# Kernel tuning notes

Hardware: AMD Instinct MI355X
Metric: run time of the kernel (lower is better)

## Reference

```python
import math
import jax, jax.numpy as jnp
import numpy as np

B, T_BI, D_BI = 64, 3000, 128
T_SW, D_SW = 375, 192
T_S1, D_S1 = 188, 192
N_FIRES = 300          # static fire count (target_lengths all = 300 -> beta = 1, ceil(sum)=300)
D_MODEL = 512
SCALE = 4.0            # scale_factor
EPS_LN = 1e-5


def _cif_integrate(h, alpha, thr, n_fires):
    """Vectorized CIF: cumsum + two scatter-adds (matches torch _cif_forward).
    h [B,T,D], alpha [B,T], thr [B,1] -> [B,n_fires,D]."""
    Bq, T, D = h.shape
    a = alpha / thr                       # normalize so boundaries sit at integers
    c = jnp.cumsum(a, axis=1)
    prev = c - a
    kp = jnp.floor(prev)
    kc = jnp.floor(c)
    fired = kc > kp                       # frame crosses a token boundary
    w_hi = jnp.where(fired, (c - kc) * thr, 0.0)          # leftover into new token
    w_lo = jnp.where(fired, (kp + 1.0 - prev) * thr, alpha)  # portion completing old token
    ip = jnp.clip(kp.astype(jnp.int32), 0, n_fires - 1)
    ic = jnp.clip(kc.astype(jnp.int32), 0, n_fires - 1)
    bidx = jnp.broadcast_to(jnp.arange(Bq)[:, None], (Bq, T))
    out = jnp.zeros((Bq, n_fires, D), h.dtype)
    out = out.at[bidx, ip].add(w_lo[..., None] * h)
    out = out.at[bidx, ic].add(w_hi[..., None] * h)
    return out


def _interp(src, t_cont, t_bi):
    """Linear interp of src [B,Ts,D] at continuous fire times t_cont [B,N] (given on the T_bi grid)."""
    Bq, Ts, D = src.shape
    t = t_cont * Ts / t_bi
    lo = jnp.clip(t.astype(jnp.int32), 0, Ts - 2)
    w = (t - lo.astype(t.dtype))[..., None]
    idx_lo = jnp.broadcast_to(lo[..., None], (Bq, t.shape[1], D))
    g_lo = jnp.take_along_axis(src, idx_lo, axis=1)
    g_hi = jnp.take_along_axis(src, idx_lo + 1, axis=1)
    return (1.0 - w) * g_lo + w * g_hi


def _forward(fire_signal, acoustic_src, acoustic_src_s1, conv_w, ln_g, ln_b, wp_w, wp_b,
             film_s0_w, film_s0_b, film_s1_w, film_s1_b, tproj_w, tproj_b,
             aproj_w, aproj_b, bproj_w, bproj_b, target_lengths):
    Bq, T_bi, _ = fire_signal.shape
    # 1) weight predictor: depthwise conv (k=1, no bias) -> LN -> Linear -> sigmoid
    x = fire_signal * conv_w                                   # depthwise 1x1 conv
    mu = jnp.mean(x, axis=-1, keepdims=True)
    var = jnp.var(x, axis=-1, keepdims=True)
    xn = (x - mu) * jax.lax.rsqrt(var + EPS_LN) * ln_g + ln_b
    alpha = SCALE * jax.nn.sigmoid(xn @ wp_w + wp_b)           # [B,T]
    tgt = target_lengths.astype(alpha.dtype)
    qty_loss = jnp.mean(jnp.abs(jnp.sum(alpha, axis=1) - tgt))
    # training-mode alpha normalization (sum alpha_cif == target)
    sum_a = jnp.clip(jnp.sum(alpha, axis=1, keepdims=True), 1e-8)
    alpha_cif = alpha * (tgt[:, None] / sum_a)
    # dynamic threshold beta = sum / ceil(sum)  (== 1 here since targets are integers)
    sum_cif = jnp.sum(alpha_cif, axis=1)
    ceil_sum = jax.lax.stop_gradient(jnp.clip(jnp.ceil(sum_cif), 1.0))
    thr = (sum_cif / ceil_sum)[:, None]                        # [B,1]
    # 2) CIF integration of temporal channel
    acoustic_temporal = _cif_integrate(fire_signal, alpha_cif, thr, N_FIRES)  # [B,N,128]
    # continuous fire times
    cum = jnp.cumsum(alpha_cif, axis=1)
    thresholds = jnp.arange(1, N_FIRES + 1, dtype=alpha.dtype)[None, :] * thr  # [B,N]
    ff = jax.vmap(jnp.searchsorted)(cum, thresholds)
    ff = jnp.minimum(ff, T_bi - 1)
    t_lo = jnp.maximum(ff - 1, 0)
    cum_at = jnp.take_along_axis(cum, t_lo, axis=1)
    a_at = jnp.take_along_axis(alpha_cif, ff, axis=1)
    t_cont = t_lo.astype(alpha.dtype) + (thresholds - cum_at) / jnp.clip(a_at, 1e-8)
    t_cont = jnp.clip(t_cont, 0.0, T_bi - 1)
    # 3) S0 pitch channel: interp + FiLM
    acoustic_pitch = _interp(acoustic_src, t_cont, T_bi)       # [B,N,192]
    film0 = acoustic_temporal @ film_s0_w + film_s0_b
    g0, b0 = jnp.split(film0, 2, axis=-1)
    pitch_mod = g0 * acoustic_pitch + b0
    # 4) project + combine
    embs = (acoustic_temporal @ tproj_w + tproj_b) + (pitch_mod @ aproj_w + aproj_b)
    # S1 beat channel
    acoustic_beat = _interp(acoustic_src_s1, t_cont, T_bi)     # [B,N,192]
    film1 = acoustic_temporal @ film_s1_w + film_s1_b
    g1, b1 = jnp.split(film1, 2, axis=-1)
    beat_mod = g1 * acoustic_beat + b1
    embs = embs + (beat_mod @ bproj_w + bproj_b)
    return embs, alpha, qty_loss


def setup_inputs() -> dict:
    key = jax.random.key(0)
    ks = jax.random.split(key, 14)
    # weight_proj bias init per module: alpha_init = target_fires/encoder_len
    p = min((128.0 / 3000.0) / SCALE, 0.99)
    wp_bias = math.log(p / (1.0 - p))
    f32 = jnp.float32
    return {
        "fire_signal": jax.random.normal(ks[0], (B, T_BI, D_BI), f32),
        "acoustic_src": jax.random.normal(ks[1], (B, T_SW, D_SW), f32),
        "acoustic_src_s1": jax.random.normal(ks[2], (B, T_S1, D_S1), f32),
        "target_lengths": jnp.full((B,), N_FIRES, jnp.int32),
        "conv_w": 1.0 + 0.1 * jax.random.normal(ks[3], (D_BI,), f32),
        "ln_g": jnp.ones((D_BI,), f32),
        "ln_b": jnp.zeros((D_BI,), f32),
        "wp_w": 0.02 * jax.random.normal(ks[4], (D_BI,), f32),
        "wp_b": jnp.asarray(wp_bias, f32),
        "film_s0_w": 0.02 * jax.random.normal(ks[5], (D_BI, 2 * D_SW), f32),
        "film_s0_b": jnp.concatenate([jnp.ones((D_SW,), f32), jnp.zeros((D_SW,), f32)]),
        "film_s1_w": 0.02 * jax.random.normal(ks[6], (D_BI, 2 * D_S1), f32),
        "film_s1_b": jnp.concatenate([jnp.ones((D_S1,), f32), jnp.zeros((D_S1,), f32)]),
        "tproj_w": 0.02 * jax.random.normal(ks[7], (D_BI, D_MODEL), f32),
        "tproj_b": jnp.zeros((D_MODEL,), f32),
        "aproj_w": 0.02 * jax.random.normal(ks[8], (D_SW, D_MODEL), f32),
        "aproj_b": jnp.zeros((D_MODEL,), f32),
        "bproj_w": 0.02 * jax.random.normal(ks[9], (D_S1, D_MODEL), f32),
        "bproj_b": jnp.zeros((D_MODEL,), f32),
    }


def reference(fire_signal, acoustic_src, acoustic_src_s1, target_lengths, conv_w, ln_g, ln_b,
              wp_w, wp_b, film_s0_w, film_s0_b, film_s1_w, film_s1_b, tproj_w, tproj_b,
              aproj_w, aproj_b, bproj_w, bproj_b):
    return _forward(fire_signal, acoustic_src, acoustic_src_s1, conv_w, ln_g, ln_b, wp_w, wp_b,
                    film_s0_w, film_s0_b, film_s1_w, film_s1_b, tproj_w, tproj_b,
                    aproj_w, aproj_b, bproj_w, bproj_b, target_lengths)
```

## Files before the change

### kernel.cpp

```cpp
#include <hip/hip_runtime.h>
#include <math.h>

#define BQ 64
#define TBI 3000
#define DBI 128
#define TSW 375
#define TS1 188
#define DSW 192
#define NF 300
#define DMODEL 512
#define EPSLN 1e-5f

typedef __bf16 bf16x8 __attribute__((ext_vector_type(8)));
typedef float f32x4 __attribute__((ext_vector_type(4)));

__device__ __forceinline__ unsigned short f2bf(float f) {
    unsigned u = __float_as_uint(f);
    unsigned r = (u + 0x7FFFu + ((u >> 16) & 1u)) >> 16;
    return (unsigned short)r;
}

__global__ __launch_bounds__(256) void k_alpha2(
    const float* __restrict__ fs, const float* __restrict__ conv_w,
    const float* __restrict__ ln_g, const float* __restrict__ ln_b,
    const float* __restrict__ wp_w, const float* __restrict__ wp_b,
    float* __restrict__ alpha_out)
{
    int wave = threadIdx.x >> 6, lane = threadIdx.x & 63;
    int l = lane & 31;
    long g = (long)blockIdx.x * 8 + wave * 2 + (lane >> 5);
    const float* row = fs + g * DBI;
    float4 f  = *(const float4*)&row[4 * l];
    float4 cw = *(const float4*)&conv_w[4 * l];
    float4 x; x.x = f.x * cw.x; x.y = f.y * cw.y; x.z = f.z * cw.z; x.w = f.w * cw.w;
    float s = x.x + x.y + x.z + x.w;
    for (int m = 16; m >= 1; m >>= 1) s += __shfl_xor(s, m, 64);
    float mu = s * (1.0f / 128.0f);
    float4 d; d.x = x.x - mu; d.y = x.y - mu; d.z = x.z - mu; d.w = x.w - mu;
    float q = d.x * d.x + d.y * d.y + d.z * d.z + d.w * d.w;
    for (int m = 16; m >= 1; m >>= 1) q += __shfl_xor(q, m, 64);
    float var = q * (1.0f / 128.0f);
    float rs = rsqrtf(var + EPSLN);
    float4 lg = *(const float4*)&ln_g[4 * l];
    float4 lb = *(const float4*)&ln_b[4 * l];
    float4 wp = *(const float4*)&wp_w[4 * l];
    float z = (d.x * rs * lg.x + lb.x) * wp.x + (d.y * rs * lg.y + lb.y) * wp.y
            + (d.z * rs * lg.z + lb.z) * wp.z + (d.w * rs * lg.w + lb.w) * wp.w;
    for (int m = 16; m >= 1; m >>= 1) z += __shfl_xor(z, m, 64);
    z += wp_b[0];
    float a = 4.0f / (1.0f + expf(-z));
    if (l == 0) alpha_out[g] = a;
}

__global__ __launch_bounds__(1024) void k_scan2(
    const float* __restrict__ alpha, const int* __restrict__ tlen,
    float2* __restrict__ params, float* __restrict__ qtyb,
    float2* __restrict__ c2, float* __restrict__ tcont)
{
    __shared__ float2 sc[TBI];
    __shared__ float2 part[2][1024];
    __shared__ double red[1024];
    int b = blockIdx.x, tid = threadIdx.x;
    const float* ar = alpha + (long)b * TBI;
    double s = 0.0;
    for (int t = tid; t < TBI; t += 1024) s += (double)ar[t];
    red[tid] = s; __syncthreads();
    for (int d = 512; d >= 1; d >>= 1) { if (tid < d) red[tid] += red[tid + d]; __syncthreads(); }
    double sum_a = red[0]; __syncthreads();
    double tgt = (double)tlen[b];
    double sa = sum_a < 1e-8 ? 1e-8 : sum_a;
    float r = (float)(tgt / sa);
    double s2 = 0.0;
    for (int t = tid; t < TBI; t += 1024) s2 += (double)(ar[t] * r);
    red[tid] = s2; __syncthreads();
    for (int d = 512; d >= 1; d >>= 1) { if (tid < d) red[tid] += red[tid + d]; __syncthreads(); }
    float sum_cif = (float)red[0];
    float cs = ceilf(sum_cif); if (cs < 1.0f) cs = 1.0f;
    float thr = sum_cif / cs;
    float rthr = 1.0f / thr;
    if (tid == 0) { params[b] = make_float2(r, thr); qtyb[b] = (float)fabs(sum_a - tgt); }
    int base = tid * 3;
    float2 run = make_float2(0.f, 0.f);
    if (base < TBI) {
        for (int j = 0; j < 3; ++j) {
            int t = base + j;
            float ac = ar[t] * r;
            run.x += ac * rthr; run.y += ac;
            sc[t] = run;
        }
    }
    part[0][tid] = (base < TBI) ? run : make_float2(0.f, 0.f);
    __syncthreads();
    int srcb = 0;
    for (int d = 1; d < 1024; d <<= 1) {
        float2 v = part[srcb][tid];
        if (tid >= d) { float2 u = part[srcb][tid - d]; v.x += u.x; v.y += u.y; }
        part[srcb ^ 1][tid] = v;
        srcb ^= 1;
        __syncthreads();
    }
    if (base < TBI && tid > 0) {
        float2 off = part[srcb][tid - 1];
        for (int j = 0; j < 3; ++j) { sc[base + j].x += off.x; sc[base + j].y += off.y; }
    }
    __syncthreads();
    for (int t = tid; t < TBI; t += 1024) {
        float ac = ar[t] * r;
        c2[(long)b * TBI + t] = make_float2(sc[t].x, ac);
    }
    if (tid < NF) {
        float v = (float)(tid + 1) * thr;
        int lo = 0, hi = TBI;
        while (lo < hi) { int mid = (lo + hi) >> 1; if (sc[mid].y < v) lo = mid + 1; else hi = mid; }
        int ff = lo; if (ff > TBI - 1) ff = TBI - 1;
        int tl = ff - 1; if (tl < 0) tl = 0;
        float cum_at = sc[tl].y;
        float a_at = ar[ff] * r;
        if (a_at < 1e-8f) a_at = 1e-8f;
        float tc = (float)tl + (v - cum_at) / a_at;
        tc = fminf(fmaxf(tc, 0.0f), (float)(TBI - 1));
        tcont[b * NF + tid] = tc;
    }
}

__global__ void k_qty(const float* __restrict__ qtyb, float* __restrict__ out)
{
    float v = qtyb[threadIdx.x & 63];
    for (int m = 32; m >= 1; m >>= 1) v += __shfl_xor(v, m, 64);
    if (threadIdx.x == 0) out[0] = v * (1.0f / (float)BQ);
}

#define FPW 94
__global__ __launch_bounds__(256) void k_cif2(
    const float* __restrict__ fs, const float2* __restrict__ c2,
    const float2* __restrict__ params, float* __restrict__ at)
{
    int wid = threadIdx.x >> 6, lane = threadIdx.x & 63;
    int wg = blockIdx.x * 4 + wid;
    int b = wg >> 5, slot = wg & 31;
    int t0 = slot * FPW;
    int t1 = t0 + FPW; if (t1 > TBI) t1 = TBI;
    if (t0 >= t1) return;
    float thr = params[b].y;
    float rthr = 1.0f / thr;
    const float2* cb = c2 + (long)b * TBI;
    const float* fb = fs + (long)b * TBI * DBI;
    float* ab = at + (long)b * NF * DBI;
    int cur = -1;
    float a0 = 0.f, a1 = 0.f;
    float2 v = cb[t0];
    float2 h = *(const float2*)&fb[(long)t0 * DBI + 2 * lane];
    for (int t = t0; t < t1; ++t) {
        float2 vn = v, hn = h;
        if (t + 1 < t1) {
            vn = cb[t + 1];
            hn = *(const float2*)&fb[(long)(t + 1) * DBI + 2 * lane];
        }
        float c = v.x, ac = v.y;
        float av = ac * rthr;
        float prev = c - av;
        float kp = floorf(prev), kc = floorf(c);
        bool fired = kc > kp;
        float w_lo = fired ? (kp + 1.0f - prev) * thr : ac;
        float w_hi = fired ? (c - kc) * thr : 0.0f;
        int ip = (int)kp; if (ip > NF - 1) ip = NF - 1; if (ip < 0) ip = 0;
        int ic = (int)kc; if (ic > NF - 1) ic = NF - 1; if (ic < 0) ic = 0;
        if (ip != cur) {
            if (cur >= 0) { atomicAdd(&ab[cur * DBI + 2 * lane], a0); atomicAdd(&ab[cur * DBI + 2 * lane + 1], a1); }
            cur = ip; a0 = 0.f; a1 = 0.f;
        }
        a0 += w_lo * h.x; a1 += w_lo * h.y;
        if (fired) {
            if (ic != cur) {
                if (cur >= 0) { atomicAdd(&ab[cur * DBI + 2 * lane], a0); atomicAdd(&ab[cur * DBI + 2 * lane + 1], a1); }
                cur = ic; a0 = 0.f; a1 = 0.f;
            }
            a0 += w_hi * h.x; a1 += w_hi * h.y;
        }
        v = vn; h = hn;
    }
    if (cur >= 0) { atomicAdd(&ab[cur * DBI + 2 * lane], a0); atomicAdd(&ab[cur * DBI + 2 * lane + 1], a1); }
}

__global__ __launch_bounds__(256) void k_prep(
    const float* __restrict__ f0w, const float* __restrict__ f1w,
    const float* __restrict__ tw, const float* __restrict__ aw, const float* __restrict__ bw,
    unsigned short* __restrict__ Wg, unsigned short* __restrict__ Wb,
    unsigned short* __restrict__ W2)
{
    int i = blockIdx.x * 256 + threadIdx.x;
    if (i < 49152) {
        int j = i & 7, lane = (i >> 3) & 63, kt = (i >> 9) & 3, nt = i >> 11;
        int k = kt * 32 + (lane >> 4) * 8 + j;
        int n = nt * 16 + (lane & 15);
        float g, b;
        if (n < 192) { g = f0w[k * 384 + n];         b = f0w[k * 384 + n + 192]; }
        else         { g = f1w[k * 384 + (n - 192)]; b = f1w[k * 384 + (n - 192) + 192]; }
        Wg[i] = f2bf(g); Wb[i] = f2bf(b);
    } else if (i < 49152 + 262144) {
        int ii = i - 49152;
        int j = ii & 7, lane = (ii >> 3) & 63, kt = (ii >> 9) & 15, nt = ii >> 13;
        int k = kt * 32 + (lane >> 4) * 8 + j;
        int n = nt * 16 + (lane & 15);
        float v;
        if (k < 128)      v = tw[k * 512 + n];
        else if (k < 320) v = aw[(k - 128) * 512 + n];
        else              v = bw[(k - 320) * 512 + n];
        W2[ii] = f2bf(v);
    }
}

__global__ void k_prepb(const float* __restrict__ f0b, const float* __restrict__ f1b,
                        const float* __restrict__ tb, const float* __restrict__ apb,
                        const float* __restrict__ bpb,
                        float* __restrict__ gbias, float* __restrict__ bbias,
                        float* __restrict__ bias2)
{
    int c = threadIdx.x;
    if (c < 384) {
        gbias[c] = c < 192 ? f0b[c] : f1b[c - 192];
        bbias[c] = c < 192 ? f0b[c + 192] : f1b[c - 192 + 192];
    }
    bias2[c] = tb[c] + apb[c] + bpb[c];
}

#define ROWS 32
__global__ __launch_bounds__(512) void k_emb4(
    const float* __restrict__ at, const float* __restrict__ tcont,
    const float* __restrict__ src0, const float* __restrict__ src1,
    const unsigned short* __restrict__ Wg, const unsigned short* __restrict__ Wb,
    const unsigned short* __restrict__ W2,
    const float* __restrict__ gbias, const float* __restrict__ bbias,
    const float* __restrict__ bias2, float* __restrict__ embs)
{
    __shared__ __align__(16) unsigned short X[ROWS][520];
    __shared__ float s_w0[ROWS], s_w1[ROWS];
    __shared__ int s_lo0[ROWS], s_lo1[ROWS], s_b[ROWS];
    int tid = threadIdx.x;
    int wave = tid >> 6, lane = tid & 63;
    long r0 = (long)blockIdx.x * ROWS;
    for (int idx = tid; idx < ROWS * 32; idx += 512) {
        int r = idx >> 5, k4 = (idx & 31) * 4;
        float4 v = *(const float4*)&at[(r0 + r) * DBI + k4];
        X[r][k4 + 0] = f2bf(v.x); X[r][k4 + 1] = f2bf(v.y);
        X[r][k4 + 2] = f2bf(v.z); X[r][k4 + 3] = f2bf(v.w);
    }
    if (tid < ROWS) {
        long g = r0 + tid;
        s_b[tid] = (int)(g / NF);
        float tc = tcont[g];
        float t0 = tc * ((float)TSW / 3000.0f);
        int lo0 = (int)t0; if (lo0 > TSW - 2) lo0 = TSW - 2; if (lo0 < 0) lo0 = 0;
        s_lo0[tid] = lo0; s_w0[tid] = t0 - (float)lo0;
        float t1 = tc * ((float)TS1 / 3000.0f);
        int lo1 = (int)t1; if (lo1 > TS1 - 2) lo1 = TS1 - 2; if (lo1 < 0) lo1 = 0;
        s_lo1[tid] = lo1; s_w1[tid] = t1 - (float)lo1;
    }
    __syncthreads();
    int mrow = lane & 15, quad = lane >> 4;
    for (int nt = wave; nt < 24; nt += 8) {
        f32x4 ag0 = {0,0,0,0}, ag1 = {0,0,0,0}, ab0 = {0,0,0,0}, ab1 = {0,0,0,0};
        #pragma unroll
        for (int kt = 0; kt < 4; ++kt) {
            bf16x8 a0 = *(const bf16x8*)&X[mrow][kt * 32 + quad * 8];
            bf16x8 a1 = *(const bf16x8*)&X[16 + mrow][kt * 32 + quad * 8];
            bf16x8 bg = *(const bf16x8*)&Wg[(((nt * 4 + kt) * 64) + lane) * 8];
            bf16x8 bb = *(const bf16x8*)&Wb[(((nt * 4 + kt) * 64) + lane) * 8];
            ag0 = __builtin_amdgcn_mfma_f32_16x16x32_bf16(a0, bg, ag0, 0, 0, 0);
            ag1 = __builtin_amdgcn_mfma_f32_16x16x32_bf16(a1, bg, ag1, 0, 0, 0);
            ab0 = __builtin_amdgcn_mfma_f32_16x16x32_bf16(a0, bb, ab0, 0, 0, 0);
            ab1 = __builtin_amdgcn_mfma_f32_16x16x32_bf16(a1, bb, ab1, 0, 0, 0);
        }
        int c = nt * 16 + mrow;
        bool sel = c >= DSW;
        int cc = sel ? c - DSW : c;
        const float* S = sel ? src1 : src0;
        int Ts = sel ? TS1 : TSW;
        float gb = gbias[c], bbv = bbias[c];
        #pragma unroll
        for (int m = 0; m < 2; ++m) {
            #pragma unroll
            for (int q = 0; q < 4; ++q) {
                int r = m * 16 + quad * 4 + q;
                int b = s_b[r];
                int lo = sel ? s_lo1[r] : s_lo0[r];
                float w = sel ? s_w1[r] : s_w0[r];
                const float* Sp = S + ((long)b * Ts + lo) * DSW + cc;
                float pv = (1.0f - w) * Sp[0] + w * Sp[DSW];
                float gv = (m ? ag1[q] : ag0[q]) + gb;
                float bv = (m ? ab1[q] : ab0[q]) + bbv;
                X[r][128 + c] = f2bf(gv * pv + bv);
            }
        }
    }
    __syncthreads();
    f32x4 acc0[4], acc1[4];
    #pragma unroll
    for (int n = 0; n < 4; ++n) { acc0[n] = (f32x4){0,0,0,0}; acc1[n] = (f32x4){0,0,0,0}; }
    for (int kt = 0; kt < 16; ++kt) {
        bf16x8 a0 = *(const bf16x8*)&X[mrow][kt * 32 + quad * 8];
        bf16x8 a1 = *(const bf16x8*)&X[16 + mrow][kt * 32 + quad * 8];
        #pragma unroll
        for (int n = 0; n < 4; ++n) {
            int nt = wave * 4 + n;
            bf16x8 bfv = *(const bf16x8*)&W2[((nt * 16 + kt) * 64 + lane) * 8];
            acc0[n] = __builtin_amdgcn_mfma_f32_16x16x32_bf16(a0, bfv, acc0[n], 0, 0, 0);
            acc1[n] = __builtin_amdgcn_mfma_f32_16x16x32_bf16(a1, bfv, acc1[n], 0, 0, 0);
        }
    }
    #pragma unroll
    for (int n = 0; n < 4; ++n) {
        int cbase = (wave * 4 + n) * 16 + mrow;
        float bv = bias2[cbase];
        #pragma unroll
        for (int q = 0; q < 4; ++q) {
            embs[(r0 + quad * 4 + q) * DMODEL + cbase] = acc0[n][q] + bv;
            embs[(r0 + 16 + quad * 4 + q) * DMODEL + cbase] = acc1[n][q] + bv;
        }
    }
}

extern "C" void kernel_launch(void* const* d_in, const int* in_sizes, int n_in,
                              void* d_out, int out_size, void* d_ws, size_t ws_size,
                              hipStream_t stream)
{
    const float* fs     = (const float*)d_in[0];
    const float* src0   = (const float*)d_in[1];
    const float* src1   = (const float*)d_in[2];
    const int*   tlen   = (const int*)d_in[3];
    const float* conv_w = (const float*)d_in[4];
    const float* ln_g   = (const float*)d_in[5];
    const float* ln_b   = (const float*)d_in[6];
    const float* wp_w   = (const float*)d_in[7];
    const float* wp_b   = (const float*)d_in[8];
    const float* f0w    = (const float*)d_in[9];
    const float* f0b    = (const float*)d_in[10];
    const float* f1w    = (const float*)d_in[11];
    const float* f1b    = (const float*)d_in[12];
    const float* tw     = (const float*)d_in[13];
    const float* tb     = (const float*)d_in[14];
    const float* aw     = (const float*)d_in[15];
    const float* apb    = (const float*)d_in[16];
    const float* bw     = (const float*)d_in[17];
    const float* bpb    = (const float*)d_in[18];

    float* embs  = (float*)d_out;
    float* alpha = embs + (long)BQ * NF * DMODEL;
    float* qtyo  = alpha + (long)BQ * TBI;

    char* ws = (char*)d_ws;
    size_t off = 0;
    float*  at     = (float*)(ws + off);  off += 9830400;
    float2* c2     = (float2*)(ws + off); off += 1536000;
    float*  tcont  = (float*)(ws + off);  off += 76800;
    float2* params = (float2*)(ws + off); off += 512;
    float*  qtyb   = (float*)(ws + off);  off += 256;
    unsigned short* Wg = (unsigned short*)(ws + off); off += 98304;
    unsigned short* Wb = (unsigned short*)(ws + off); off += 98304;
    unsigned short* W2 = (unsigned short*)(ws + off); off += 524288;
    float* gbias = (float*)(ws + off); off += 1536;
    float* bbias = (float*)(ws + off); off += 1536;
    float* bias2 = (float*)(ws + off); off += 2048;

    hipMemsetAsync(at, 0, (size_t)BQ * NF * DBI * sizeof(float), stream);
    k_prep<<<1216, 256, 0, stream>>>(f0w, f1w, tw, aw, bw, Wg, Wb, W2);
    k_prepb<<<1, 512, 0, stream>>>(f0b, f1b, tb, apb, bpb, gbias, bbias, bias2);
    k_alpha2<<<(BQ * TBI) / 8, 256, 0, stream>>>(fs, conv_w, ln_g, ln_b, wp_w, wp_b, alpha);
    k_scan2<<<BQ, 1024, 0, stream>>>(alpha, tlen, params, qtyb, c2, tcont);
    k_qty<<<1, 64, 0, stream>>>(qtyb, qtyo);
    k_cif2<<<512, 256, 0, stream>>>(fs, c2, params, at);
    k_emb4<<<(BQ * NF) / ROWS, 512, 0, stream>>>(at, tcont, src0, src1,
                                                 Wg, Wb, W2, gbias, bbias, bias2, embs);
}
```

Baseline: 297.4 us.

## Partition CIF by output tokens to drop atomics and memset, merge small launches

```diff
diff --git a/kernel.cpp b/kernel.cpp
--- a/kernel.cpp
+++ b/kernel.cpp
@@ -52,10 +52,10 @@
     if (l == 0) alpha_out[g] = a;
 }
 
-__global__ __launch_bounds__(1024) void k_scan2(
+__global__ __launch_bounds__(1024) void k_scan3(
     const float* __restrict__ alpha, const int* __restrict__ tlen,
-    float2* __restrict__ params, float* __restrict__ qtyb,
-    float2* __restrict__ c2, float* __restrict__ tcont)
+    float2* __restrict__ params, float* __restrict__ qtyo,
+    float2* __restrict__ c2, float* __restrict__ tcont, int* __restrict__ ffout)
 {
     __shared__ float2 sc[TBI];
     __shared__ float2 part[2][1024];
@@ -78,7 +78,10 @@
     float cs = ceilf(sum_cif); if (cs < 1.0f) cs = 1.0f;
     float thr = sum_cif / cs;
     float rthr = 1.0f / thr;
-    if (tid == 0) { params[b] = make_float2(r, thr); qtyb[b] = (float)fabs(sum_a - tgt); }
+    if (tid == 0) {
+        params[b] = make_float2(r, thr);
+        atomicAdd(qtyo, (float)fabs(sum_a - tgt) * (1.0f / (float)BQ));
+    }
     int base = tid * 3;
     float2 run = make_float2(0.f, 0.f);
     if (base < TBI) {
@@ -113,6 +116,7 @@
         int lo = 0, hi = TBI;
         while (lo < hi) { int mid = (lo + hi) >> 1; if (sc[mid].y < v) lo = mid + 1; else hi = mid; }
         int ff = lo; if (ff > TBI - 1) ff = TBI - 1;
+        ffout[b * NF + tid] = ff;
         int tl = ff - 1; if (tl < 0) tl = 0;
         float cum_at = sc[tl].y;
         float a_at = ar[ff] * r;
@@ -123,39 +127,35 @@
     }
 }
 
-__global__ void k_qty(const float* __restrict__ qtyb, float* __restrict__ out)
-{
-    float v = qtyb[threadIdx.x & 63];
-    for (int m = 32; m >= 1; m >>= 1) v += __shfl_xor(v, m, 64);
-    if (threadIdx.x == 0) out[0] = v * (1.0f / (float)BQ);
-}
-
-#define FPW 94
-__global__ __launch_bounds__(256) void k_cif2(
+#define TPW 3
+__global__ __launch_bounds__(256) void k_cif3(
     const float* __restrict__ fs, const float2* __restrict__ c2,
-    const float2* __restrict__ params, float* __restrict__ at)
+    const int* __restrict__ ffA, const float2* __restrict__ params,
+    float* __restrict__ at)
 {
     int wid = threadIdx.x >> 6, lane = threadIdx.x & 63;
     int wg = blockIdx.x * 4 + wid;
-    int b = wg >> 5, slot = wg & 31;
-    int t0 = slot * FPW;
-    int t1 = t0 + FPW; if (t1 > TBI) t1 = TBI;
-    if (t0 >= t1) return;
+    int b = wg / 100, slot = wg - b * 100;
+    int j0 = slot * TPW;
+    const int* ffb = ffA + b * NF;
+    int t0 = (j0 == 0) ? 0 : ffb[j0 - 1];
+    int tE = (slot == 99) ? (TBI - 1) : ffb[j0 + TPW - 1];
     float thr = params[b].y;
     float rthr = 1.0f / thr;
     const float2* cb = c2 + (long)b * TBI;
     const float* fb = fs + (long)b * TBI * DBI;
     float* ab = at + (long)b * NF * DBI;
+    int nw = j0;
     int cur = -1;
     float a0 = 0.f, a1 = 0.f;
-    float2 v = cb[t0];
-    float2 h = *(const float2*)&fb[(long)t0 * DBI + 2 * lane];
-    for (int t = t0; t < t1; ++t) {
-        float2 vn = v, hn = h;
-        if (t + 1 < t1) {
-            vn = cb[t + 1];
-            hn = *(const float2*)&fb[(long)(t + 1) * DBI + 2 * lane];
-        }
+    #define FLUSH() do { \
+        if (cur >= j0 && cur < j0 + TPW) { \
+            while (nw < cur) { *(float2*)&ab[nw * DBI + 2 * lane] = make_float2(0.f, 0.f); ++nw; } \
+            *(float2*)&ab[cur * DBI + 2 * lane] = make_float2(a0, a1); nw = cur + 1; \
+        } } while (0)
+    for (int t = t0; t <= tE; ++t) {
+        float2 v = cb[t];
+        float2 h = *(const float2*)&fb[(long)t * DBI + 2 * lane];
         float c = v.x, ac = v.y;
         float av = ac * rthr;
         float prev = c - av;
@@ -165,29 +165,39 @@
         float w_hi = fired ? (c - kc) * thr : 0.0f;
         int ip = (int)kp; if (ip > NF - 1) ip = NF - 1; if (ip < 0) ip = 0;
         int ic = (int)kc; if (ic > NF - 1) ic = NF - 1; if (ic < 0) ic = 0;
-        if (ip != cur) {
-            if (cur >= 0) { atomicAdd(&ab[cur * DBI + 2 * lane], a0); atomicAdd(&ab[cur * DBI + 2 * lane + 1], a1); }
-            cur = ip; a0 = 0.f; a1 = 0.f;
-        }
+        if (ip != cur) { FLUSH(); cur = ip; a0 = 0.f; a1 = 0.f; }
         a0 += w_lo * h.x; a1 += w_lo * h.y;
         if (fired) {
-            if (ic != cur) {
-                if (cur >= 0) { atomicAdd(&ab[cur * DBI + 2 * lane], a0); atomicAdd(&ab[cur * DBI + 2 * lane + 1], a1); }
-                cur = ic; a0 = 0.f; a1 = 0.f;
-            }
+            if (ic != cur) { FLUSH(); cur = ic; a0 = 0.f; a1 = 0.f; }
             a0 += w_hi * h.x; a1 += w_hi * h.y;
         }
-        v = vn; h = hn;
-    }
-    if (cur >= 0) { atomicAdd(&ab[cur * DBI + 2 * lane], a0); atomicAdd(&ab[cur * DBI + 2 * lane + 1], a1); }
-}
-
-__global__ __launch_bounds__(256) void k_prep(
+    }
+    FLUSH();
+    while (nw < j0 + TPW) { *(float2*)&ab[nw * DBI + 2 * lane] = make_float2(0.f, 0.f); ++nw; }
+    #undef FLUSH
+}
+
+__global__ __launch_bounds__(256) void k_prep2(
     const float* __restrict__ f0w, const float* __restrict__ f1w,
     const float* __restrict__ tw, const float* __restrict__ aw, const float* __restrict__ bw,
+    const float* __restrict__ f0b, const float* __restrict__ f1b,
+    const float* __restrict__ tb, const float* __restrict__ apb, const float* __restrict__ bpb,
     unsigned short* __restrict__ Wg, unsigned short* __restrict__ Wb,
-    unsigned short* __restrict__ W2)
-{
+    unsigned short* __restrict__ W2,
+    float* __restrict__ gbias, float* __restrict__ bbias, float* __restrict__ bias2,
+    float* __restrict__ qtyo)
+{
+    if (blockIdx.x == 1216) {
+        for (int c = threadIdx.x; c < 512; c += 256) {
+            if (c < 384) {
+                gbias[c] = c < 192 ? f0b[c] : f1b[c - 192];
+                bbias[c] = c < 192 ? f0b[c + 192] : f1b[c - 192 + 192];
+            }
+            bias2[c] = tb[c] + apb[c] + bpb[c];
+        }
+        if (threadIdx.x == 0) qtyo[0] = 0.f;
+        return;
+    }
     int i = blockIdx.x * 256 + threadIdx.x;
     if (i < 49152) {
         int j = i & 7, lane = (i >> 3) & 63, kt = (i >> 9) & 3, nt = i >> 11;
@@ -197,7 +207,7 @@
         if (n < 192) { g = f0w[k * 384 + n];         b = f0w[k * 384 + n + 192]; }
         else         { g = f1w[k * 384 + (n - 192)]; b = f1w[k * 384 + (n - 192) + 192]; }
         Wg[i] = f2bf(g); Wb[i] = f2bf(b);
-    } else if (i < 49152 + 262144) {
+    } else {
         int ii = i - 49152;
         int j = ii & 7, lane = (ii >> 3) & 63, kt = (ii >> 9) & 15, nt = ii >> 13;
         int k = kt * 32 + (lane >> 4) * 8 + j;
@@ -210,22 +220,8 @@
     }
 }
 
-__global__ void k_prepb(const float* __restrict__ f0b, const float* __restrict__ f1b,
-                        const float* __restrict__ tb, const float* __restrict__ apb,
-                        const float* __restrict__ bpb,
-                        float* __restrict__ gbias, float* __restrict__ bbias,
-                        float* __restrict__ bias2)
-{
-    int c = threadIdx.x;
-    if (c < 384) {
-        gbias[c] = c < 192 ? f0b[c] : f1b[c - 192];
-        bbias[c] = c < 192 ? f0b[c + 192] : f1b[c - 192 + 192];
-    }
-    bias2[c] = tb[c] + apb[c] + bpb[c];
-}
-
-#define ROWS 32
-__global__ __launch_bounds__(512) void k_emb4(
+#define EROWS 16
+__global__ __launch_bounds__(512, 6) void k_emb5(
     const float* __restrict__ at, const float* __restrict__ tcont,
     const float* __restrict__ src0, const float* __restrict__ src1,
     const unsigned short* __restrict__ Wg, const unsigned short* __restrict__ Wb,
@@ -233,19 +229,19 @@
     const float* __restrict__ gbias, const float* __restrict__ bbias,
     const float* __restrict__ bias2, float* __restrict__ embs)
 {
-    __shared__ __align__(16) unsigned short X[ROWS][520];
-    __shared__ float s_w0[ROWS], s_w1[ROWS];
-    __shared__ int s_lo0[ROWS], s_lo1[ROWS], s_b[ROWS];
+    __shared__ __align__(16) unsigned short X[EROWS][520];
+    __shared__ float s_w0[EROWS], s_w1[EROWS];
+    __shared__ int s_lo0[EROWS], s_lo1[EROWS], s_b[EROWS];
     int tid = threadIdx.x;
     int wave = tid >> 6, lane = tid & 63;
-    long r0 = (long)blockIdx.x * ROWS;
-    for (int idx = tid; idx < ROWS * 32; idx += 512) {
-        int r = idx >> 5, k4 = (idx & 31) * 4;
+    long r0 = (long)blockIdx.x * EROWS;
+    {
+        int r = tid >> 5, k4 = (tid & 31) * 4;
         float4 v = *(const float4*)&at[(r0 + r) * DBI + k4];
         X[r][k4 + 0] = f2bf(v.x); X[r][k4 + 1] = f2bf(v.y);
         X[r][k4 + 2] = f2bf(v.z); X[r][k4 + 3] = f2bf(v.w);
     }
-    if (tid < ROWS) {
+    if (tid < EROWS) {
         long g = r0 + tid;
         s_b[tid] = (int)(g / NF);
         float tc = tcont[g];
@@ -259,17 +255,14 @@
     __syncthreads();
     int mrow = lane & 15, quad = lane >> 4;
     for (int nt = wave; nt < 24; nt += 8) {
-        f32x4 ag0 = {0,0,0,0}, ag1 = {0,0,0,0}, ab0 = {0,0,0,0}, ab1 = {0,0,0,0};
+        f32x4 ag = {0,0,0,0}, ab = {0,0,0,0};
         #pragma unroll
         for (int kt = 0; kt < 4; ++kt) {
-            bf16x8 a0 = *(const bf16x8*)&X[mrow][kt * 32 + quad * 8];
-            bf16x8 a1 = *(const bf16x8*)&X[16 + mrow][kt * 32 + quad * 8];
+            bf16x8 a = *(const bf16x8*)&X[mrow][kt * 32 + quad * 8];
             bf16x8 bg = *(const bf16x8*)&Wg[(((nt * 4 + kt) * 64) + lane) * 8];
             bf16x8 bb = *(const bf16x8*)&Wb[(((nt * 4 + kt) * 64) + lane) * 8];
-            ag0 = __builtin_amdgcn_mfma_f32_16x16x32_bf16(a0, bg, ag0, 0, 0, 0);
-            ag1 = __builtin_amdgcn_mfma_f32_16x16x32_bf16(a1, bg, ag1, 0, 0, 0);
-            ab0 = __builtin_amdgcn_mfma_f32_16x16x32_bf16(a0, bb, ab0, 0, 0, 0);
-            ab1 = __builtin_amdgcn_mfma_f32_16x16x32_bf16(a1, bb, ab1, 0, 0, 0);
+            ag = __builtin_amdgcn_mfma_f32_16x16x32_bf16(a, bg, ag, 0, 0, 0);
+            ab = __builtin_amdgcn_mfma_f32_16x16x32_bf16(a, bb, ab, 0, 0, 0);
         }
         int c = nt * 16 + mrow;
         bool sel = c >= DSW;
@@ -278,34 +271,27 @@
         int Ts = sel ? TS1 : TSW;
         float gb = gbias[c], bbv = bbias[c];
         #pragma unroll
-        for (int m = 0; m < 2; ++m) {
-            #pragma unroll
-            for (int q = 0; q < 4; ++q) {
-                int r = m * 16 + quad * 4 + q;
-                int b = s_b[r];
-                int lo = sel ? s_lo1[r] : s_lo0[r];
-                float w = sel ? s_w1[r] : s_w0[r];
-                const float* Sp = S + ((long)b * Ts + lo) * DSW + cc;
-                float pv = (1.0f - w) * Sp[0] + w * Sp[DSW];
-                float gv = (m ? ag1[q] : ag0[q]) + gb;
-                float bv = (m ? ab1[q] : ab0[q]) + bbv;
-                X[r][128 + c] = f2bf(gv * pv + bv);
-            }
+        for (int q = 0; q < 4; ++q) {
+            int r = quad * 4 + q;
+            int b = s_b[r];
+            int lo = sel ? s_lo1[r] : s_lo0[r];
+            float w = sel ? s_w1[r] : s_w0[r];
+            const float* Sp = S + ((long)b * Ts + lo) * DSW + cc;
+            float pv = (1.0f - w) * Sp[0] + w * Sp[DSW];
+            X[r][128 + c] = f2bf((ag[q] + gb) * pv + (ab[q] + bbv));
         }
     }
     __syncthreads();
-    f32x4 acc0[4], acc1[4];
+    f32x4 acc[4];
     #pragma unroll
-    for (int n = 0; n < 4; ++n) { acc0[n] = (f32x4){0,0,0,0}; acc1[n] = (f32x4){0,0,0,0}; }
+    for (int n = 0; n < 4; ++n) acc[n] = (f32x4){0, 0, 0, 0};
     for (int kt = 0; kt < 16; ++kt) {
-        bf16x8 a0 = *(const bf16x8*)&X[mrow][kt * 32 + quad * 8];
-        bf16x8 a1 = *(const bf16x8*)&X[16 + mrow][kt * 32 + quad * 8];
+        bf16x8 a = *(const bf16x8*)&X[mrow][kt * 32 + quad * 8];
         #pragma unroll
         for (int n = 0; n < 4; ++n) {
             int nt = wave * 4 + n;
             bf16x8 bfv = *(const bf16x8*)&W2[((nt * 16 + kt) * 64 + lane) * 8];
-            acc0[n] = __builtin_amdgcn_mfma_f32_16x16x32_bf16(a0, bfv, acc0[n], 0, 0, 0);
-            acc1[n] = __builtin_amdgcn_mfma_f32_16x16x32_bf16(a1, bfv, acc1[n], 0, 0, 0);
+            acc[n] = __builtin_amdgcn_mfma_f32_16x16x32_bf16(a, bfv, acc[n], 0, 0, 0);
         }
     }
     #pragma unroll
@@ -313,10 +299,8 @@
         int cbase = (wave * 4 + n) * 16 + mrow;
         float bv = bias2[cbase];
         #pragma unroll
-        for (int q = 0; q < 4; ++q) {
-            embs[(r0 + quad * 4 + q) * DMODEL + cbase] = acc0[n][q] + bv;
-            embs[(r0 + 16 + quad * 4 + q) * DMODEL + cbase] = acc1[n][q] + bv;
-        }
+        for (int q = 0; q < 4; ++q)
+            embs[(r0 + quad * 4 + q) * DMODEL + cbase] = acc[n][q] + bv;
     }
 }
 
@@ -353,8 +337,8 @@
     float*  at     = (float*)(ws + off);  off += 9830400;
     float2* c2     = (float2*)(ws + off); off += 1536000;
     float*  tcont  = (float*)(ws + off);  off += 76800;
+    int*    ffA    = (int*)(ws + off);    off += 76800;
     float2* params = (float2*)(ws + off); off += 512;
-    float*  qtyb   = (float*)(ws + off);  off += 256;
     unsigned short* Wg = (unsigned short*)(ws + off); off += 98304;
     unsigned short* Wb = (unsigned short*)(ws + off); off += 98304;
     unsigned short* W2 = (unsigned short*)(ws + off); off += 524288;
@@ -362,13 +346,11 @@
     float* bbias = (float*)(ws + off); off += 1536;
     float* bias2 = (float*)(ws + off); off += 2048;
 
-    hipMemsetAsync(at, 0, (size_t)BQ * NF * DBI * sizeof(float), stream);
-    k_prep<<<1216, 256, 0, stream>>>(f0w, f1w, tw, aw, bw, Wg, Wb, W2);
-    k_prepb<<<1, 512, 0, stream>>>(f0b, f1b, tb, apb, bpb, gbias, bbias, bias2);
+    k_prep2<<<1217, 256, 0, stream>>>(f0w, f1w, tw, aw, bw, f0b, f1b, tb, apb, bpb,
+                                      Wg, Wb, W2, gbias, bbias, bias2, qtyo);
     k_alpha2<<<(BQ * TBI) / 8, 256, 0, stream>>>(fs, conv_w, ln_g, ln_b, wp_w, wp_b, alpha);
-    k_scan2<<<BQ, 1024, 0, stream>>>(alpha, tlen, params, qtyb, c2, tcont);
-    k_qty<<<1, 64, 0, stream>>>(qtyb, qtyo);
-    k_cif2<<<512, 256, 0, stream>>>(fs, c2, params, at);
-    k_emb4<<<(BQ * NF) / ROWS, 512, 0, stream>>>(at, tcont, src0, src1,
-                                                 Wg, Wb, W2, gbias, bbias, bias2, embs);
-}
+    k_scan3<<<BQ, 1024, 0, stream>>>(alpha, tlen, params, qtyo, c2, tcont, ffA);
+    k_cif3<<<(BQ * 100) / 4, 256, 0, stream>>>(fs, c2, ffA, params, at);
+    k_emb5<<<(BQ * NF) / EROWS, 512, 0, stream>>>(at, tcont, src0, src1,
+                                                  Wg, Wb, W2, gbias, bbias, bias2, embs);
+}
```

Result: faster. 275.2 us (-7.5%).
